# Kernel tuning notes

Hardware: AMD Instinct MI355X
Metric: run time of the kernel (lower is better)

## Reference

```python
import jax, jax.numpy as jnp
import numpy as np


def _sample_level(tables, gx, gy, align_corners):
    # tables: [3, C, H, W]; gx, gy: [3, P] grid coords in [-1, 1]
    # emulates F.grid_sample(mode='bilinear', padding_mode='border')
    def one(tab, x, y):
        C, H, W = tab.shape
        if align_corners:
            ix = (x + 1.0) * 0.5 * (W - 1)
            iy = (y + 1.0) * 0.5 * (H - 1)
        else:
            ix = ((x + 1.0) * W - 1.0) * 0.5
            iy = ((y + 1.0) * H - 1.0) * 0.5
        ix = jnp.clip(ix, 0.0, W - 1.0)  # border padding
        iy = jnp.clip(iy, 0.0, H - 1.0)
        x0 = jnp.floor(ix)
        y0 = jnp.floor(iy)
        wx = ix - x0
        wy = iy - y0
        x0i = x0.astype(jnp.int32)
        y0i = y0.astype(jnp.int32)
        x1i = jnp.minimum(x0i + 1, W - 1)
        y1i = jnp.minimum(y0i + 1, H - 1)
        v00 = tab[:, y0i, x0i]  # [C, P]
        v01 = tab[:, y0i, x1i]
        v10 = tab[:, y1i, x0i]
        v11 = tab[:, y1i, x1i]
        top = v00 * (1.0 - wx) + v01 * wx
        bot = v10 * (1.0 - wx) + v11 * wx
        return (top * (1.0 - wy) + bot * wy).T  # [P, C]

    return jax.vmap(one, in_axes=(0, 0, 0))(tables, gx, gy)  # [3, P, C]


def _hexplane(xyz, t, bounds, sps, tps):
    lead = xyz.shape[:-1]
    xyz = xyz.reshape(-1, 3)
    t = t.reshape(-1, t.shape[-1])
    xyzn = (xyz - bounds[:, 0, :]) / (bounds[:, 1, :] - bounds[:, 0, :])
    x, y, z = xyzn[:, 0], xyzn[:, 1], xyzn[:, 2]
    # spatial planes: xy, xz, yz; grid[...,0]->W, grid[...,1]->H
    sgx = jnp.stack([x, x, y]) * 2.0 - 1.0  # [3, P]
    sgy = jnp.stack([y, z, z]) * 2.0 - 1.0
    tt = t[:, 0]
    # temporal planes: (t, x), (t, y), (t, z); t -> W (dim_time), coord -> H (res)
    tgx = jnp.stack([tt, tt, tt]) * 2.0 - 1.0
    tgy = jnp.stack([x, y, z]) * 2.0 - 1.0
    sfeat = jnp.concatenate([_sample_level(sp, sgx, sgy, False) for sp in sps], axis=-1)  # [3, P, C*L]
    tfeat = jnp.concatenate([_sample_level(tp, tgx, tgy, True) for tp in tps], axis=-1)   # [3, P, C*L]
    feat = jnp.concatenate([sfeat, tfeat], axis=0)  # [6, P, C*L]
    val = jnp.transpose(feat, (1, 0, 2)).reshape(feat.shape[1], -1)  # [P, 6*C*L]
    return val.reshape(*lead, val.shape[-1])


def setup_inputs() -> dict:
    key = jax.random.key(0)
    N = 1_000_000
    C = 8
    T = 100
    STD = 0.1
    resolutions = [16, 32, 64, 128]
    ks = jax.random.split(key, 2 + 2 * len(resolutions))
    xyz = jax.random.uniform(ks[0], (N, 3), dtype=jnp.float32)
    t = jax.random.uniform(ks[1], (N, 1), dtype=jnp.float32)
    bounds = jnp.stack([jnp.zeros((1, 3), jnp.float32), jnp.ones((1, 3), jnp.float32)], axis=1)  # [1, 2, 3]
    inp = {"xyz": xyz, "t": t, "bounds": bounds}
    for i, r in enumerate(resolutions):
        inp[f"sp{i}"] = jax.random.uniform(ks[2 + i], (3, C, r, r), jnp.float32, -STD, STD)
        inp[f"tp{i}"] = jax.random.uniform(ks[2 + len(resolutions) + i], (3, C, r, T), jnp.float32, -STD, STD)
    return inp


def reference(xyz, t, bounds, sp0, sp1, sp2, sp3, tp0, tp1, tp2, tp3):
    return _hexplane(xyz, t, bounds, (sp0, sp1, sp2, sp3), (tp0, tp1, tp2, tp3))
```

## Files before the change

kernel.cpp:

```cpp
#include <hip/hip_runtime.h>
#include <hip/hip_bf16.h>

typedef float f32x2 __attribute__((ext_vector_type(2)));
typedef float f32x4 __attribute__((ext_vector_type(4)));
typedef unsigned int u32;
typedef u32 u32x4 __attribute__((ext_vector_type(4)));

#define EXP_SP0 0
#define EXP_SP1 24576
#define EXP_SP2 122880
#define EXP_TP0 516096
#define EXP_TP1 669696
#define PL_SP3  976896
#define PL_TP2  1370112
#define PL_TP3  1523712

__global__ __launch_bounds__(256) void build_tabs(
    const float* __restrict__ sp0, const float* __restrict__ sp1,
    const float* __restrict__ sp2, const float* __restrict__ sp3,
    const float* __restrict__ tp0, const float* __restrict__ tp1,
    const float* __restrict__ tp2, const float* __restrict__ tp3,
    unsigned short* __restrict__ dst)
{
    int tab = blockIdx.y;
    const float* src; int W, H, off; bool ex;
    switch (tab) {
        case 0: src = sp0; W = 16;  H = 16;  off = EXP_SP0; ex = true;  break;
        case 1: src = sp1; W = 32;  H = 32;  off = EXP_SP1; ex = true;  break;
        case 2: src = sp2; W = 64;  H = 64;  off = EXP_SP2; ex = true;  break;
        case 3: src = tp0; W = 100; H = 16;  off = EXP_TP0; ex = true;  break;
        case 4: src = tp1; W = 100; H = 32;  off = EXP_TP1; ex = true;  break;
        case 5: src = sp3; W = 128; H = 128; off = PL_SP3;  ex = false; break;
        case 6: src = tp2; W = 100; H = 64;  off = PL_TP2;  ex = false; break;
        default:src = tp3; W = 100; H = 128; off = PL_TP3;  ex = false; break;
    }
    int HW = W * H;
    int per = ex ? 32 : 8;
    int total = 3 * HW * per;
    int i = blockIdx.x * 256 + threadIdx.x;
    if (i >= total) return;

    int q = i / per;
    int x  = q % W;
    int y  = (q / W) % H;
    int pl = q / HW;

    int c, xk, yk;
    if (ex) {
        int u = i & 31, d = u >> 1, half = u & 1;
        c  = d & 7;
        xk = min(x + half, W - 1);
        yk = (d >> 3) ? min(y + 1, H - 1) : y;
    } else {
        c = i & 7; xk = x; yk = y;
    }
    float v = src[(size_t)(pl * 8 + c) * HW + (size_t)yk * W + xk];
    __hip_bfloat16 b = __float2bfloat16(v);
    dst[off + i] = *reinterpret_cast<unsigned short*>(&b);
}

__device__ __forceinline__ float dot2bf(u32 ab, u32 w, float acc) {
    float d;
    asm("v_dot2_f32_bf16 %0, %1, %2, %3" : "=v"(d) : "v"(ab), "v"(w), "v"(acc));
    return d;
}
__device__ __forceinline__ u32 pk_bf16(float lo, float hi) {
    u32 d;
    asm("v_cvt_pk_bf16_f32 %0, %1, %2" : "=v"(d) : "v"(lo), "v"(hi));
    return d;
}

__global__ __launch_bounds__(192) void hexplane_dot2(
    const float* __restrict__ xyz, const float* __restrict__ t,
    const float* __restrict__ bounds, const unsigned short* __restrict__ tw,
    float* __restrict__ out, int N)
{
    __shared__ float coords[8][4];
    __shared__ float ostage[1536];

    int tid = threadIdx.x;
    int n0  = blockIdx.x * 8;

    if (tid < 32) {
        int p = tid >> 2, comp = tid & 3;
        int n = n0 + p;
        float v = 0.0f;
        if (n < N) {
            if (comp < 3) {
                float b0 = bounds[comp], b1 = bounds[3 + comp];
                v = (xyz[(size_t)n * 3 + comp] - b0) / (b1 - b0);
            } else {
                v = t[n];
            }
        }
        coords[p][comp] = v;
    }
    __syncthreads();

    int p = tid / 24;
    int s = tid - p * 24;
    int g = s >> 2;
    int r = s & 3;
    int res = 16 << r;

    f32x4 cd = *(f32x4*)&coords[p][0];
    float xn = cd[0], yn = cd[1], zn = cd[2], tt = cd[3];

    int W, H;
    float ix, iy;
    bool ex;
    int base;
    if (g < 3) {
        W = res; H = res;
        ex = (r < 3);
        if (ex) {
            int lo = (r==0) ? EXP_SP0 : (r==1) ? EXP_SP1 : EXP_SP2;
            base = lo + g * res * res * 32;
        } else {
            base = PL_SP3 + g * 128 * 128 * 8;
        }
        float fx = (g==2) ? yn : xn;
        float fy = (g==0) ? yn : zn;
        ix = fx * (float)W - 0.5f;
        iy = fy * (float)H - 0.5f;
    } else {
        int q = g - 3;
        W = 100; H = res;
        ex = (r < 2);
        if (ex) {
            int lo = (r==0) ? EXP_TP0 : EXP_TP1;
            base = lo + q * res * 100 * 32;
        } else {
            int lo = (r==2) ? PL_TP2 : PL_TP3;
            base = lo + q * res * 100 * 8;
        }
        float fy = (q==0) ? xn : (q==1) ? yn : zn;
        ix = tt * 99.0f;
        iy = fy * (float)(H - 1);
    }

    ix = fminf(fmaxf(ix, 0.0f), (float)(W - 1));
    iy = fminf(fmaxf(iy, 0.0f), (float)(H - 1));
    float x0f = floorf(ix), y0f = floorf(iy);
    float wx = ix - x0f, wy = iy - y0f;
    int x0 = (int)x0f, y0 = (int)y0f;

    float omx = 1.0f - wx, omy = 1.0f - wy;
    u32 wT = pk_bf16(omx * omy, wx * omy);
    u32 wB = pk_bf16(omx * wy,  wx * wy);

    u32 top[8], bot[8];
    if (ex) {
        const u32x4* ep = (const u32x4*)(tw + base + (size_t)(y0 * W + x0) * 32);
        u32x4 t0 = ep[0], t1 = ep[1], b0 = ep[2], b1 = ep[3];
        #pragma unroll
        for (int k = 0; k < 4; ++k) { top[k] = t0[k]; top[4+k] = t1[k]; }
        #pragma unroll
        for (int k = 0; k < 4; ++k) { bot[k] = b0[k]; bot[4+k] = b1[k]; }
    } else {
        int x1 = min(x0 + 1, W - 1), y1 = min(y0 + 1, H - 1);
        const unsigned short* tb = tw + base;
        u32x4 c00 = *(const u32x4*)(tb + (size_t)(y0*W + x0) * 8);
        u32x4 c01 = *(const u32x4*)(tb + (size_t)(y0*W + x1) * 8);
        u32x4 c10 = *(const u32x4*)(tb + (size_t)(y1*W + x0) * 8);
        u32x4 c11 = *(const u32x4*)(tb + (size_t)(y1*W + x1) * 8);
        #pragma unroll
        for (int k = 0; k < 4; ++k) {
            top[2*k]   = __builtin_amdgcn_perm(c00[k], c01[k], 0x01000504u);
            top[2*k+1] = __builtin_amdgcn_perm(c00[k], c01[k], 0x03020706u);
            bot[2*k]   = __builtin_amdgcn_perm(c10[k], c11[k], 0x01000504u);
            bot[2*k+1] = __builtin_amdgcn_perm(c10[k], c11[k], 0x03020706u);
        }
    }

    float f[8];
    #pragma unroll
    for (int c = 0; c < 8; ++c) {
        float a = dot2bf(top[c], wT, 0.0f);
        f[c] = dot2bf(bot[c], wB, a);
    }

    {
        int q = (tid >> 2) & 3;
        #pragma unroll
        for (int j = 0; j < 4; ++j) {
            f32x2 w2 = { f[2*j], f[2*j+1] };
            *(f32x2*)&ostage[tid * 8 + (j ^ q) * 2] = w2;
        }
    }
    __syncthreads();

    size_t total_out = (size_t)N * 192;
    int a = tid & 1;

    int e0 = tid >> 1;
    int q0 = (e0 >> 2) & 3;
    int sg0 = a ^ (q0 >> 1);
    f32x4 v0 = *(f32x4*)&ostage[e0 * 8 + sg0 * 4];
    if (q0 & 1) { f32x4 tmp = { v0[2], v0[3], v0[0], v0[1] }; v0 = tmp; }

    int e1 = 96 + (tid >> 1);
    int q1 = (e1 >> 2) & 3;
    int sg1 = a ^ (q1 >> 1);
    f32x4 v1 = *(f32x4*)&ostage[e1 * 8 + sg1 * 4];
    if (q1 & 1) { f32x4 tmp = { v1[2], v1[3], v1[0], v1[1] }; v1 = tmp; }

    size_t F0 = (size_t)n0 * 192 + (size_t)tid * 4;
    size_t F1 = F0 + 768;
    if (F0 + 4 <= total_out)
        __builtin_nontemporal_store(v0, (f32x4*)(out + F0));
    if (F1 + 4 <= total_out)
        __builtin_nontemporal_store(v1, (f32x4*)(out + F1));
}

extern "C" void kernel_launch(void* const* d_in, const int* in_sizes, int n_in,
                              void* d_out, int out_size, void* d_ws, size_t ws_size,
                              hipStream_t stream) {
    const float* xyz    = (const float*)d_in[0];
    const float* t      = (const float*)d_in[1];
    const float* bounds = (const float*)d_in[2];
    const float* sp[4]  = { (const float*)d_in[3], (const float*)d_in[5],
                            (const float*)d_in[7], (const float*)d_in[9] };
    const float* tp[4]  = { (const float*)d_in[4], (const float*)d_in[6],
                            (const float*)d_in[8], (const float*)d_in[10] };
    float* out = (float*)d_out;

    int N = in_sizes[0] / 3;
    unsigned short* tw = (unsigned short*)d_ws;

    build_tabs<<<dim3(1536, 8), 256, 0, stream>>>(
        sp[0], sp[1], sp[2], sp[3], tp[0], tp[1], tp[2], tp[3], tw);

    int blocks = (N + 7) / 8;
    hexplane_dot2<<<blocks, 192, 0, stream>>>(xyz, t, bounds, tw, out, N);
}
```

Measured before the change: 242.5 us.

## Expand all tables to packed corner layout and drive sampling with shared LUT

Every table, including the largest spatial and temporal levels, is now stored in the expanded 4-corner bf16 layout, so each sample does one contiguous 64-byte load instead of four scattered loads plus permutes. Per-lane plane parameters (scales, offsets, clamps, base offset, coordinate selectors) are precomputed into a small shared-memory LUT, which removes divergent branching in the main kernel. The cost is a build pass that is about four times larger and a bigger workspace footprint, which may hurt cache locality for the large tables.

```diff
diff --git a/kernel.cpp b/kernel.cpp
--- a/kernel.cpp
+++ b/kernel.cpp
@@ -6,14 +6,14 @@
 typedef unsigned int u32;
 typedef u32 u32x4 __attribute__((ext_vector_type(4)));
 
-#define EXP_SP0 0
-#define EXP_SP1 24576
-#define EXP_SP2 122880
-#define EXP_TP0 516096
-#define EXP_TP1 669696
-#define PL_SP3  976896
-#define PL_TP2  1370112
-#define PL_TP3  1523712
+#define E_SP0 0
+#define E_SP1 24576
+#define E_SP2 122880
+#define E_SP3 516096
+#define E_TP0 2088960
+#define E_TP1 2242560
+#define E_TP2 2549760
+#define E_TP3 3164160
 
 __global__ __launch_bounds__(256) void build_tabs(
     const float* __restrict__ sp0, const float* __restrict__ sp1,
@@ -23,37 +23,34 @@
     unsigned short* __restrict__ dst)
 {
     int tab = blockIdx.y;
-    const float* src; int W, H, off; bool ex;
-    switch (tab) {
-        case 0: src = sp0; W = 16;  H = 16;  off = EXP_SP0; ex = true;  break;
-        case 1: src = sp1; W = 32;  H = 32;  off = EXP_SP1; ex = true;  break;
-        case 2: src = sp2; W = 64;  H = 64;  off = EXP_SP2; ex = true;  break;
-        case 3: src = tp0; W = 100; H = 16;  off = EXP_TP0; ex = true;  break;
-        case 4: src = tp1; W = 100; H = 32;  off = EXP_TP1; ex = true;  break;
-        case 5: src = sp3; W = 128; H = 128; off = PL_SP3;  ex = false; break;
-        case 6: src = tp2; W = 100; H = 64;  off = PL_TP2;  ex = false; break;
-        default:src = tp3; W = 100; H = 128; off = PL_TP3;  ex = false; break;
-    }
+    int r = tab & 3;
+    bool is_tp = tab >= 4;
+    int res = 16 << r;
+    int W = is_tp ? 100 : res;
+    int H = res;
     int HW = W * H;
-    int per = ex ? 32 : 8;
-    int total = 3 * HW * per;
+    int total = 3 * HW * 32;
     int i = blockIdx.x * 256 + threadIdx.x;
     if (i >= total) return;
 
-    int q = i / per;
+    const float* src =
+        (tab==0) ? sp0 : (tab==1) ? sp1 : (tab==2) ? sp2 : (tab==3) ? sp3 :
+        (tab==4) ? tp0 : (tab==5) ? tp1 : (tab==6) ? tp2 : tp3;
+    int off =
+        (tab==0) ? E_SP0 : (tab==1) ? E_SP1 : (tab==2) ? E_SP2 : (tab==3) ? E_SP3 :
+        (tab==4) ? E_TP0 : (tab==5) ? E_TP1 : (tab==6) ? E_TP2 : E_TP3;
+
+    int u    = i & 31;
+    int d    = u >> 1;
+    int half = u & 1;
+    int c    = d & 7;
+    int row  = d >> 3;
+    int q  = i >> 5;
     int x  = q % W;
     int y  = (q / W) % H;
     int pl = q / HW;
-
-    int c, xk, yk;
-    if (ex) {
-        int u = i & 31, d = u >> 1, half = u & 1;
-        c  = d & 7;
-        xk = min(x + half, W - 1);
-        yk = (d >> 3) ? min(y + 1, H - 1) : y;
-    } else {
-        c = i & 7; xk = x; yk = y;
-    }
+    int xk = min(x + half, W - 1);
+    int yk = row ? min(y + 1, H - 1) : y;
     float v = src[(size_t)(pl * 8 + c) * HW + (size_t)yk * W + xk];
     __hip_bfloat16 b = __float2bfloat16(v);
     dst[off + i] = *reinterpret_cast<unsigned short*>(&b);
@@ -70,12 +67,14 @@
     return d;
 }
 
-__global__ __launch_bounds__(192) void hexplane_dot2(
+__global__ __launch_bounds__(192) void hexplane_lut(
     const float* __restrict__ xyz, const float* __restrict__ t,
     const float* __restrict__ bounds, const unsigned short* __restrict__ tw,
     float* __restrict__ out, int N)
 {
     __shared__ float coords[8][4];
+    __shared__ f32x4 lutA[24];
+    __shared__ f32x4 lutB[24];
     __shared__ float ostage[1536];
 
     int tid = threadIdx.x;
@@ -94,53 +93,59 @@
             }
         }
         coords[p][comp] = v;
+    } else if (tid >= 64 && tid < 88) {
+        int s = tid - 64;
+        int g = s >> 2;
+        int r = s & 3;
+        int res = 16 << r;
+        float sx, ox, sy, oy, cx, cy;
+        int base, W, selx, sely;
+        if (g < 3) {
+            W = res;
+            sx = (float)res; ox = -0.5f;
+            sy = (float)res; oy = -0.5f;
+            cx = (float)(res - 1); cy = (float)(res - 1);
+            int lo = (r==0) ? E_SP0 : (r==1) ? E_SP1 : (r==2) ? E_SP2 : E_SP3;
+            base = lo + g * res * res * 32;
+            selx = (g==2) ? 1 : 0;
+            sely = (g==0) ? 1 : 2;
+        } else {
+            int q = g - 3;
+            W = 100;
+            sx = 99.0f; ox = 0.0f;
+            sy = (float)(res - 1); oy = 0.0f;
+            cx = 99.0f; cy = (float)(res - 1);
+            int lo = (r==0) ? E_TP0 : (r==1) ? E_TP1 : (r==2) ? E_TP2 : E_TP3;
+            base = lo + q * res * 100 * 32;
+            selx = 3;
+            sely = q;
+        }
+        f32x4 A = { sx, ox, sy, oy };
+        f32x4 B = { cx, cy,
+                    __int_as_float(base * 2),
+                    __int_as_float(W | (selx << 8) | (sely << 12)) };
+        lutA[s] = A;
+        lutB[s] = B;
     }
     __syncthreads();
 
     int p = tid / 24;
     int s = tid - p * 24;
-    int g = s >> 2;
-    int r = s & 3;
-    int res = 16 << r;
-
-    f32x4 cd = *(f32x4*)&coords[p][0];
-    float xn = cd[0], yn = cd[1], zn = cd[2], tt = cd[3];
-
-    int W, H;
-    float ix, iy;
-    bool ex;
-    int base;
-    if (g < 3) {
-        W = res; H = res;
-        ex = (r < 3);
-        if (ex) {
-            int lo = (r==0) ? EXP_SP0 : (r==1) ? EXP_SP1 : EXP_SP2;
-            base = lo + g * res * res * 32;
-        } else {
-            base = PL_SP3 + g * 128 * 128 * 8;
-        }
-        float fx = (g==2) ? yn : xn;
-        float fy = (g==0) ? yn : zn;
-        ix = fx * (float)W - 0.5f;
-        iy = fy * (float)H - 0.5f;
-    } else {
-        int q = g - 3;
-        W = 100; H = res;
-        ex = (r < 2);
-        if (ex) {
-            int lo = (r==0) ? EXP_TP0 : EXP_TP1;
-            base = lo + q * res * 100 * 32;
-        } else {
-            int lo = (r==2) ? PL_TP2 : PL_TP3;
-            base = lo + q * res * 100 * 8;
-        }
-        float fy = (q==0) ? xn : (q==1) ? yn : zn;
-        ix = tt * 99.0f;
-        iy = fy * (float)(H - 1);
-    }
-
-    ix = fminf(fmaxf(ix, 0.0f), (float)(W - 1));
-    iy = fminf(fmaxf(iy, 0.0f), (float)(H - 1));
+
+    f32x4 A = lutA[s];
+    f32x4 B = lutB[s];
+    int code = __float_as_int(B[3]);
+    int W    = code & 255;
+    int selx = (code >> 8) & 15;
+    int sely = (code >> 12) & 15;
+
+    float fx = coords[p][selx];
+    float fy = coords[p][sely];
+
+    float ix = fmaf(fx, A[0], A[1]);
+    float iy = fmaf(fy, A[2], A[3]);
+    ix = fminf(fmaxf(ix, 0.0f), B[0]);
+    iy = fminf(fmaxf(iy, 0.0f), B[1]);
     float x0f = floorf(ix), y0f = floorf(iy);
     float wx = ix - x0f, wy = iy - y0f;
     int x0 = (int)x0f, y0 = (int)y0f;
@@ -149,35 +154,20 @@
     u32 wT = pk_bf16(omx * omy, wx * omy);
     u32 wB = pk_bf16(omx * wy,  wx * wy);
 
-    u32 top[8], bot[8];
-    if (ex) {
-        const u32x4* ep = (const u32x4*)(tw + base + (size_t)(y0 * W + x0) * 32);
-        u32x4 t0 = ep[0], t1 = ep[1], b0 = ep[2], b1 = ep[3];
-        #pragma unroll
-        for (int k = 0; k < 4; ++k) { top[k] = t0[k]; top[4+k] = t1[k]; }
-        #pragma unroll
-        for (int k = 0; k < 4; ++k) { bot[k] = b0[k]; bot[4+k] = b1[k]; }
-    } else {
-        int x1 = min(x0 + 1, W - 1), y1 = min(y0 + 1, H - 1);
-        const unsigned short* tb = tw + base;
-        u32x4 c00 = *(const u32x4*)(tb + (size_t)(y0*W + x0) * 8);
-        u32x4 c01 = *(const u32x4*)(tb + (size_t)(y0*W + x1) * 8);
-        u32x4 c10 = *(const u32x4*)(tb + (size_t)(y1*W + x0) * 8);
-        u32x4 c11 = *(const u32x4*)(tb + (size_t)(y1*W + x1) * 8);
-        #pragma unroll
-        for (int k = 0; k < 4; ++k) {
-            top[2*k]   = __builtin_amdgcn_perm(c00[k], c01[k], 0x01000504u);
-            top[2*k+1] = __builtin_amdgcn_perm(c00[k], c01[k], 0x03020706u);
-            bot[2*k]   = __builtin_amdgcn_perm(c10[k], c11[k], 0x01000504u);
-            bot[2*k+1] = __builtin_amdgcn_perm(c10[k], c11[k], 0x03020706u);
-        }
-    }
+    int ebyte = __float_as_int(B[2]) + (y0 * W + x0) * 64;
+    const u32x4* ep = (const u32x4*)((const char*)tw + ebyte);
+    u32x4 t0 = ep[0];
+    u32x4 t1 = ep[1];
+    u32x4 b0 = ep[2];
+    u32x4 b1 = ep[3];
 
     float f[8];
     #pragma unroll
-    for (int c = 0; c < 8; ++c) {
-        float a = dot2bf(top[c], wT, 0.0f);
-        f[c] = dot2bf(bot[c], wB, a);
+    for (int k = 0; k < 4; ++k) {
+        float a  = dot2bf(t0[k], wT, 0.0f);
+        f[k]     = dot2bf(b0[k], wB, a);
+        float a2 = dot2bf(t1[k], wT, 0.0f);
+        f[4+k]   = dot2bf(b1[k], wB, a2);
     }
 
     {
@@ -228,9 +218,9 @@
     int N = in_sizes[0] / 3;
     unsigned short* tw = (unsigned short*)d_ws;
 
-    build_tabs<<<dim3(1536, 8), 256, 0, stream>>>(
+    build_tabs<<<dim3(6144, 8), 256, 0, stream>>>(
         sp[0], sp[1], sp[2], sp[3], tp[0], tp[1], tp[2], tp[3], tw);
 
     int blocks = (N + 7) / 8;
-    hexplane_dot2<<<blocks, 192, 0, stream>>>(xyz, t, bounds, tw, out, N);
-}
+    hexplane_lut<<<blocks, 192, 0, stream>>>(xyz, t, bounds, tw, out, N);
+}
```

After: 286.8 us. 18.3% more time.
